# Performance work log

Measured on AMD Instinct MI355X. Metric: run time of the kernel, lower is better.

Reference implementation:

```python
import jax, jax.numpy as jnp
import numpy as np


def setup_inputs() -> dict:
    key = jax.random.key(0)
    k0, k1, k2, k3 = jax.random.split(key, 4)
    B, C = 32, 768
    t_h = t_w = 8
    s_h = s_w = 16
    N = t_h * t_w * 2 + s_h * s_w  # 384
    return {
        "x_v": jax.random.normal(k0, (B, N, C), jnp.float32),
        "x_i": jax.random.normal(k1, (B, N, C), jnp.float32),
        "qkv_w": jax.random.normal(k2, (3 * C, C), jnp.float32) * 0.02,
        "proj_w": jax.random.normal(k3, (C, C), jnp.float32) * 0.02,
        "proj_b": jnp.zeros((C,), jnp.float32),
        "t_h": t_h, "t_w": t_w, "s_h": s_h, "s_w": s_w,
        "num_heads": 12,
    }


def reference(x_v, x_i, qkv_w, proj_w, proj_b, t_h, t_w, s_h, s_w, num_heads):
    B, N, C = x_v.shape
    H = num_heads
    Dh = C // H
    scale = Dh ** (-0.5)
    mt = t_h * t_w * 2  # template tokens (two templates)

    # joint QKV projection over both modalities: [2B, N, C]
    x = jnp.concatenate([x_v, x_i], axis=0)
    qkv = (x @ qkv_w.T).reshape(2 * B, N, 3, H, Dh)
    qkv = jnp.transpose(qkv, (2, 0, 3, 1, 4))  # [3, 2B, H, N, Dh]
    q, k, v = qkv[0], qkv[1], qkv[2]
    qV, qI = q[:B], q[B:]
    kV, kI = k[:B], k[B:]
    vV, vI = v[:B], v[B:]

    q_mt_V, q_s_V = qV[:, :, :mt], qV[:, :, mt:]
    k_mt_V, k_s_V = kV[:, :, :mt], kV[:, :, mt:]
    v_mt_V, v_s_V = vV[:, :, :mt], vV[:, :, mt:]
    q_mt_I, q_s_I = qI[:, :, :mt], qI[:, :, mt:]
    k_mt_I, k_s_I = kI[:, :, :mt], kI[:, :, mt:]
    v_mt_I, v_s_I = vI[:, :, :mt], vI[:, :, mt:]

    # shared cross-modal template KV
    k_mt = jnp.concatenate([k_mt_V, k_mt_I], axis=2)
    v_mt = jnp.concatenate([v_mt_V, v_mt_I], axis=2)

    def attend(q_, k_, v_):
        a = jax.nn.softmax(jnp.einsum('bhqd,bhkd->bhqk', q_, k_) * scale, axis=-1)
        o = jnp.einsum('bhqk,bhkd->bhqd', a, v_)
        return o.transpose(0, 2, 1, 3).reshape(B, -1, C)

    # template branches: self-attention within own modality
    x_mt_V = attend(q_mt_V, k_mt_V, v_mt_V)
    x_mt_I = attend(q_mt_I, k_mt_I, v_mt_I)
    # search branches: attend to cross-modal templates + own search
    x_s_V = attend(q_s_V, jnp.concatenate([k_mt, k_s_V], axis=2),
                   jnp.concatenate([v_mt, v_s_V], axis=2))
    x_s_I = attend(q_s_I, jnp.concatenate([k_mt, k_s_I], axis=2),
                   jnp.concatenate([v_mt, v_s_I], axis=2))

    x_V = jnp.concatenate([x_mt_V, x_s_V], axis=1)
    x_I = jnp.concatenate([x_mt_I, x_s_I], axis=1)
    out = jnp.concatenate([x_V, x_I], axis=0) @ proj_w.T + proj_b
    return out[:B], out[B:]
```

## Files before the change

### kernel.cpp

```cpp
#include <hip/hip_runtime.h>

typedef __bf16 bf16;
typedef __bf16 bf16x4 __attribute__((ext_vector_type(4)));
typedef __bf16 bf16x8 __attribute__((ext_vector_type(8)));
typedef float f32x4 __attribute__((ext_vector_type(4)));

#define MFMA16(a,b,c) __builtin_amdgcn_mfma_f32_16x16x32_bf16((a),(b),(c),0,0,0)
#define SBAR() __builtin_amdgcn_s_barrier()
#define SCHED0() __builtin_amdgcn_sched_barrier(0)
#define EXP2(x) __builtin_amdgcn_exp2f(x)


__device__ inline void gload16(const bf16* g, bf16* l) {
  __builtin_amdgcn_global_load_lds(
      (const __attribute__((address_space(1))) void*)g,
      (__attribute__((address_space(3))) void*)l, 16, 0, 0);
}

__device__ inline void stage128(const bf16* __restrict__ gsrc,
                                bf16* lds_base, int tid, int wv) {
#pragma unroll
  for (int r = 0; r < 4; ++r) {
    int s = r * 256 + tid;
    int row = s >> 3;
    int chunk = (s & 7) ^ (row & 7);
    gload16(gsrc + (size_t)row * 768 + chunk * 8,
            lds_base + (size_t)(r * 256 + wv * 64) * 8);
  }
}

__device__ inline bf16x8 frag64(const bf16* buf, int row, int ks, int lg) {
  int slot = ((ks << 2) | lg) ^ (row & 7);
  return *(const bf16x8*)(buf + (size_t)row * 64 + slot * 8);
}

#define GEMM128_LOOP(APANEL, BPANEL, NTILES)                                    \
  do {                                                                          \
    stage128((APANEL), &As[0][0][0], tid, wv);                                  \
    stage128((BPANEL), &Bs[0][0][0], tid, wv);                                  \
    stage128((APANEL) + 64, &As[1][0][0], tid, wv);                             \
    stage128((BPANEL) + 64, &Bs[1][0][0], tid, wv);                             \
    asm volatile("s_waitcnt vmcnt(8)" ::: "memory"); SCHED0();                  \
    SBAR();                                                                     \
    int c = 0;                                                                  \
    for (int t = 0; t < (NTILES); ++t) {                                        \
      const bf16* Ab = &As[c][0][0];                                            \
      const bf16* Bb = &Bs[c][0][0];                                            \
      bf16x8 af[4][2], bfr[4][2];                                               \
      _Pragma("unroll")                                                         \
      for (int nf = 0; nf < 4; ++nf)                                            \
        _Pragma("unroll")                                                       \
        for (int ks = 0; ks < 2; ++ks)                                          \
          bfr[nf][ks] = frag64(Bb, wc + nf * 16 + lr, ks, lg);                  \
      _Pragma("unroll")                                                         \
      for (int mf = 0; mf < 4; ++mf)                                            \
        _Pragma("unroll")                                                       \
        for (int ks = 0; ks < 2; ++ks)                                          \
          af[mf][ks] = frag64(Ab, wr + mf * 16 + lr, ks, lg);                   \
      asm volatile("s_waitcnt lgkmcnt(0)" ::: "memory"); SCHED0();              \
      SBAR();              \
      if (t + 2 < (NTILES)) {                                                   \
        stage128((APANEL) + (t + 2) * 64, &As[c][0][0], tid, wv);               \
        stage128((BPANEL) + (t + 2) * 64, &Bs[c][0][0], tid, wv);               \
      }                                                                         \
      __builtin_amdgcn_s_setprio(1);                                            \
      _Pragma("unroll")                                                         \
      for (int mf = 0; mf < 4; ++mf)                                            \
        _Pragma("unroll")                                                       \
        for (int nf = 0; nf < 4; ++nf)                                          \
          _Pragma("unroll")                                                     \
          for (int ks = 0; ks < 2; ++ks)                                        \
            acc[mf][nf] = MFMA16(af[mf][ks], bfr[nf][ks], acc[mf][nf]);         \
      __builtin_amdgcn_s_setprio(0);                                            \
      if (t + 2 < (NTILES)) { asm volatile("s_waitcnt vmcnt(8)" ::: "memory"); }\
      else                  { asm volatile("s_waitcnt vmcnt(0)" ::: "memory"); }\
      SCHED0();                                                                 \
      SBAR();                       \
      c ^= 1;                                                                   \
    }                                                                           \
  } while (0)

__global__ __launch_bounds__(256) void convert1_kernel(
    const float* __restrict__ xv, const float* __restrict__ xi,
    const float* __restrict__ w, bf16* __restrict__ dst)
{
  const size_t NV = 9437184;
  const size_t NX = 18874368;
  const size_t NT = 20643840;
  for (size_t i = (size_t)blockIdx.x * 256 + threadIdx.x; i * 8 < NT;
       i += (size_t)gridDim.x * 256) {
    size_t e = i * 8;
    const float* src;
    if (e < NV)      src = xv + e;
    else if (e < NX) src = xi + (e - NV);
    else             src = w + (e - NX);
    f32x4 a = *(const f32x4*)src;
    f32x4 b = *(const f32x4*)(src + 4);
    bf16x8 r;
    r[0] = (bf16)a[0]; r[1] = (bf16)a[1]; r[2] = (bf16)a[2]; r[3] = (bf16)a[3];
    r[4] = (bf16)b[0]; r[5] = (bf16)b[1]; r[6] = (bf16)b[2]; r[7] = (bf16)b[3];
    *(bf16x8*)(dst + e) = r;
  }
}

__global__ __launch_bounds__(256) void convert2_kernel(
    const float* __restrict__ w, bf16* __restrict__ dst)
{
  size_t i = (size_t)blockIdx.x * 256 + threadIdx.x;
  size_t e = i * 8;
  if (e >= 589824) return;
  f32x4 a = *(const f32x4*)(w + e);
  f32x4 b = *(const f32x4*)(w + e + 4);
  bf16x8 r;
  r[0] = (bf16)a[0]; r[1] = (bf16)a[1]; r[2] = (bf16)a[2]; r[3] = (bf16)a[3];
  r[4] = (bf16)b[0]; r[5] = (bf16)b[1]; r[6] = (bf16)b[2]; r[7] = (bf16)b[3];
  *(bf16x8*)(dst + e) = r;
}

__global__ __launch_bounds__(256, 2) void qkv_kernel(
    const bf16* __restrict__ X, const bf16* __restrict__ W,
    bf16* __restrict__ Qo, bf16* __restrict__ Ko, bf16* __restrict__ VTo)
{
  __shared__ union {
    struct { bf16 A[2][128][64]; bf16 B[2][128][64]; } k;
    bf16 ep[128][132];
  } lds;
  bf16 (&As)[2][128][64] = lds.k.A;
  bf16 (&Bs)[2][128][64] = lds.k.B;

  int bid = blockIdx.x;
  int swz = (bid & 7) * 432 + (bid >> 3);
  const int nt = swz % 18, mt = swz / 18;
  const int m0 = mt * 128, n0 = nt * 128;
  const int tid = threadIdx.x;
  const int lane = tid & 63;
  const int wv = tid >> 6;
  const int wr = (wv >> 1) * 64, wc = (wv & 1) * 64;
  const int lr = lane & 15, lg = lane >> 4;

  const bf16* Xp = X + (size_t)m0 * 768;
  const bf16* Wp = W + (size_t)n0 * 768;

  f32x4 acc[4][4] = {};

  GEMM128_LOOP(Xp, Wp, 12);

  const int comp = nt / 6;
  if (comp == 2) {
#pragma unroll
    for (int mf = 0; mf < 4; ++mf)
#pragma unroll
      for (int nf = 0; nf < 4; ++nf) {
        int m = m0 + wr + mf * 16 + lg * 4;
        int n = n0 + wc + nf * 16 + lr;
        int bp = m / 384, tok = m - bp * 384;
        int rem = n - 1536;
        int hh = rem >> 6, d = rem & 63;
        bf16x4 pk;
        pk[0] = (bf16)acc[mf][nf][0]; pk[1] = (bf16)acc[mf][nf][1];
        pk[2] = (bf16)acc[mf][nf][2]; pk[3] = (bf16)acc[mf][nf][3];
        *(bf16x4*)(VTo + (((size_t)bp * 12 + hh) * 64 + d) * 384 + tok) = pk;
      }
  } else {
    const float scl = (comp == 0) ? 0.18033688f : 1.0f;
#pragma unroll
    for (int mf = 0; mf < 4; ++mf)
#pragma unroll
      for (int nf = 0; nf < 4; ++nf)
#pragma unroll
        for (int r = 0; r < 4; ++r)
          lds.ep[wr + mf * 16 + lg * 4 + r][wc + nf * 16 + lr] =
              (bf16)(acc[mf][nf][r] * scl);
    __syncthreads();
    bf16* dst = (comp == 0) ? Qo : Ko;
    const int nb = n0 - comp * 768;
#pragma unroll
    for (int it = 0; it < 8; ++it) {
      int idx = it * 256 + tid;
      int row = idx >> 4, ch = idx & 15;
      int m = m0 + row;
      int bp = m / 384, tok = m - bp * 384;
      int rem = nb + ch * 8;
      int hh = rem >> 6, d = rem & 63;
      *(bf16x8*)(dst + (((size_t)bp * 12 + hh) * 384 + tok) * 64 + d) =
          *(const bf16x8*)(&lds.ep[row][ch * 8]);
    }
  }
}

__global__ __launch_bounds__(256) void attn_kernel(
    const bf16* __restrict__ Q, const bf16* __restrict__ K, const bf16* __restrict__ VT,
    bf16* __restrict__ ATT)
{
  __shared__ union {
    bf16 Qs[128][72];
    bf16 Ps[4][32][136];
  } u;
  __shared__ bf16 Ks[128][72];
  __shared__ bf16 VTs[64][136];

  const int bid = blockIdx.x;
  const int qb = bid % 3;
  const int h  = (bid / 3) % 12;
  const int bp = bid / 36;
  const int tid = threadIdx.x;
  const int lane = tid & 63;
  const int wv = tid >> 6;
  const int lr = lane & 15, lg = lane >> 4;

  const size_t bh384 = ((size_t)bp * 12 + h) * 384;
  const int q0 = qb * 128;
  const int nchunks = (qb == 0) ? 1 : 4;

  auto chunk_base = [&](int c, size_t& kb, size_t& vtb) {
    int src_b, t0;
    if (qb == 0)      { src_b = bp;             t0 = 0; }
    else if (c == 0)  { src_b = bp & 31;        t0 = 0; }
    else if (c == 1)  { src_b = (bp & 31) + 32; t0 = 0; }
    else              { src_b = bp;             t0 = (c - 1) * 128; }
    kb  = (((size_t)src_b * 12 + h) * 384 + t0) * 64;
    vtb = ((size_t)src_b * 12 + h) * 64 * 384 + t0;
  };

  for (int v = tid; v < 1024; v += 256) {
    int row = v >> 3, cg = (v & 7) * 8;
    *(bf16x8*)(&u.Qs[row][cg]) = *(const bf16x8*)(Q + (bh384 + q0 + row) * 64 + cg);
  }
  __syncthreads();

  bf16x8 qf[2][2];
#pragma unroll
  for (int mf = 0; mf < 2; ++mf)
#pragma unroll
    for (int ks = 0; ks < 2; ++ks)
      qf[mf][ks] = *(const bf16x8*)(&u.Qs[wv * 32 + mf * 16 + lr][ks * 32 + lg * 8]);

  const int krow = tid >> 3,  kcg = (tid & 7) * 8;
  const int vd   = tid >> 4,  vp  = (tid & 15) * 8;
  bf16x8 kreg[4], vreg[4];
  {
    size_t kb, vtb; chunk_base(0, kb, vtb);
#pragma unroll
    for (int i = 0; i < 4; ++i) {
      kreg[i] = *(const bf16x8*)(K + kb + (size_t)(krow + i * 32) * 64 + kcg);
      vreg[i] = *(const bf16x8*)(VT + vtb + (size_t)(vd + i * 16) * 384 + vp);
    }
  }

  f32x4 O[2][4] = {};
  float runmax[2] = {-1e30f, -1e30f}, runsum[2] = {0.f, 0.f};

  for (int c = 0; c < nchunks; ++c) {
    __syncthreads();
#pragma unroll
    for (int i = 0; i < 4; ++i) {
      *(bf16x8*)(&Ks[krow + i * 32][kcg]) = kreg[i];
      *(bf16x8*)(&VTs[vd + i * 16][vp])   = vreg[i];
    }
    __syncthreads();

    if (c + 1 < nchunks) {
      size_t kb, vtb; chunk_base(c + 1, kb, vtb);
#pragma unroll
      for (int i = 0; i < 4; ++i) {
        kreg[i] = *(const bf16x8*)(K + kb + (size_t)(krow + i * 32) * 64 + kcg);
        vreg[i] = *(const bf16x8*)(VT + vtb + (size_t)(vd + i * 16) * 384 + vp);
      }
    }

    f32x4 St[2][8] = {};
#pragma unroll
    for (int nf = 0; nf < 8; ++nf) {
#pragma unroll
      for (int ks = 0; ks < 2; ++ks) {
        bf16x8 kf = *(const bf16x8*)(&Ks[nf * 16 + lr][ks * 32 + lg * 8]);
        St[0][nf] = MFMA16(kf, qf[0][ks], St[0][nf]);
        St[1][nf] = MFMA16(kf, qf[1][ks], St[1][nf]);
      }
    }

    float rfq[2];
#pragma unroll
    for (int mf = 0; mf < 2; ++mf) {
      float m4[8];
#pragma unroll
      for (int nf = 0; nf < 8; ++nf)
        m4[nf] = fmaxf(fmaxf(St[mf][nf][0], St[mf][nf][1]),
                       fmaxf(St[mf][nf][2], St[mf][nf][3]));
      float mx = fmaxf(fmaxf(fmaxf(m4[0], m4[1]), fmaxf(m4[2], m4[3])),
                       fmaxf(fmaxf(m4[4], m4[5]), fmaxf(m4[6], m4[7])));
      mx = fmaxf(mx, __shfl_xor(mx, 16));
      mx = fmaxf(mx, __shfl_xor(mx, 32));
      float nm = fmaxf(runmax[mf], mx);
      rfq[mf] = EXP2(runmax[mf] - nm);
      runmax[mf] = nm;
      float s4[8];
#pragma unroll
      for (int nf = 0; nf < 8; ++nf) {
        St[mf][nf][0] = EXP2(St[mf][nf][0] - nm);
        St[mf][nf][1] = EXP2(St[mf][nf][1] - nm);
        St[mf][nf][2] = EXP2(St[mf][nf][2] - nm);
        St[mf][nf][3] = EXP2(St[mf][nf][3] - nm);
        s4[nf] = (St[mf][nf][0] + St[mf][nf][1]) + (St[mf][nf][2] + St[mf][nf][3]);
      }
      float rs = ((s4[0] + s4[1]) + (s4[2] + s4[3])) +
                 ((s4[4] + s4[5]) + (s4[6] + s4[7]));
      rs += __shfl_xor(rs, 16);
      rs += __shfl_xor(rs, 32);
      runsum[mf] = runsum[mf] * rfq[mf] + rs;
    }

#pragma unroll
    for (int mf = 0; mf < 2; ++mf)
#pragma unroll
      for (int nf = 0; nf < 8; ++nf) {
        bf16x4 pk;
        pk[0] = (bf16)St[mf][nf][0]; pk[1] = (bf16)St[mf][nf][1];
        pk[2] = (bf16)St[mf][nf][2]; pk[3] = (bf16)St[mf][nf][3];
        *(bf16x4*)(&u.Ps[wv][mf * 16 + lr][nf * 16 + lg * 4]) = pk;
      }

#pragma unroll
    for (int mf = 0; mf < 2; ++mf)
#pragma unroll
      for (int r = 0; r < 4; ++r) {
        float rr = __shfl(rfq[mf], (lg * 4 + r) + (lg << 4));
#pragma unroll
        for (int vn = 0; vn < 4; ++vn) O[mf][vn][r] *= rr;
      }

#pragma unroll
    for (int ks = 0; ks < 4; ++ks) {
      bf16x8 pf0 = *(const bf16x8*)(&u.Ps[wv][lr][ks * 32 + lg * 8]);
      bf16x8 pf1 = *(const bf16x8*)(&u.Ps[wv][16 + lr][ks * 32 + lg * 8]);
#pragma unroll
      for (int vn = 0; vn < 4; ++vn) {
        bf16x8 vf = *(const bf16x8*)(&VTs[vn * 16 + lr][ks * 32 + lg * 8]);
        O[0][vn] = MFMA16(pf0, vf, O[0][vn]);
        O[1][vn] = MFMA16(pf1, vf, O[1][vn]);
      }
    }
  }

#pragma unroll
  for (int mf = 0; mf < 2; ++mf) {
#pragma unroll
    for (int r = 0; r < 4; ++r) {
      float rs = __shfl(runsum[mf], (lg * 4 + r) + (lg << 4));
      float inv = 1.0f / rs;
#pragma unroll
      for (int vn = 0; vn < 4; ++vn) {
        int tok = q0 + wv * 32 + mf * 16 + lg * 4 + r;
        int d = vn * 16 + lr;
        ATT[((size_t)bp * 384 + tok) * 768 + h * 64 + d] = (bf16)(O[mf][vn][r] * inv);
      }
    }
  }
}

__global__ __launch_bounds__(256, 2) void proj_kernel(
    const bf16* __restrict__ A, const bf16* __restrict__ W,
    const float* __restrict__ bias, float* __restrict__ out)
{
  __shared__ bf16 As[2][128][64];
  __shared__ bf16 Bs[2][128][64];
  int bid = blockIdx.x;
  int swz = (bid & 7) * 144 + (bid >> 3);
  const int nt = swz % 6, mt = swz / 6;
  const int m0 = mt * 128, n0 = nt * 128;
  const int tid = threadIdx.x;
  const int lane = tid & 63;
  const int wv = tid >> 6;
  const int wr = (wv >> 1) * 64, wc = (wv & 1) * 64;
  const int lr = lane & 15, lg = lane >> 4;

  const bf16* Ap = A + (size_t)m0 * 768;
  const bf16* Wpp = W + (size_t)n0 * 768;

  f32x4 acc[4][4] = {};

  GEMM128_LOOP(Ap, Wpp, 12);

#pragma unroll
  for (int mf = 0; mf < 4; ++mf)
#pragma unroll
    for (int nf = 0; nf < 4; ++nf)
#pragma unroll
      for (int r = 0; r < 4; ++r) {
        int m = m0 + wr + mf * 16 + lg * 4 + r;
        int n = n0 + wc + nf * 16 + lr;
        out[(size_t)m * 768 + n] = acc[mf][nf][r] + bias[n];
      }
}

extern "C" void kernel_launch(void* const* d_in, const int* in_sizes, int n_in,
                              void* d_out, int out_size, void* d_ws, size_t ws_size,
                              hipStream_t stream) {
  (void)in_sizes; (void)n_in; (void)out_size; (void)ws_size;
  const float* xv     = (const float*)d_in[0];
  const float* xi     = (const float*)d_in[1];
  const float* qkv_w  = (const float*)d_in[2];
  const float* proj_w = (const float*)d_in[3];
  const float* proj_b = (const float*)d_in[4];
  float* out = (float*)d_out;

  bf16* Xb = (bf16*)d_out;
  bf16* Wq = Xb + (size_t)18874368;

  const size_t SZ = (size_t)64 * 12 * 384 * 64;
  bf16* Q   = (bf16*)d_ws;
  bf16* K   = Q + SZ;
  bf16* VT  = K + SZ;
  bf16* ATT = VT + SZ;
  bf16* Wp  = Q;

  convert1_kernel<<<2048, 256, 0, stream>>>(xv, xi, qkv_w, Xb);
  qkv_kernel<<<3456, 256, 0, stream>>>(Xb, Wq, Q, K, VT);
  attn_kernel<<<64 * 12 * 3, 256, 0, stream>>>(Q, K, VT, ATT);
  convert2_kernel<<<288, 256, 0, stream>>>(proj_w, Wp);
  proj_kernel<<<1152, 256, 0, stream>>>(ATT, Wp, proj_b, out);
}
```

Measured before the change: 244.2 us.

## Fuse fp32-to-bf16 activation conversion into QKV GEMM A-tile loading

```diff
diff --git a/kernel.cpp b/kernel.cpp
--- a/kernel.cpp
+++ b/kernel.cpp
@@ -33,6 +33,27 @@
   int slot = ((ks << 2) | lg) ^ (row & 7);
   return *(const bf16x8*)(buf + (size_t)row * 64 + slot * 8);
 }
+
+#define A_ISSUE(KT)                                                             \
+  _Pragma("unroll")                                                             \
+  for (int i = 0; i < 8; ++i) {                                                 \
+    int s = i * 256 + tid;                                                      \
+    int row = s >> 4, c4 = (s & 15) * 4;                                        \
+    areg[i] = *(const f32x4*)(Asrc + (size_t)row * 768 + (KT) + c4);            \
+  }
+
+#define A_WRITE(BUFA)                                                           \
+  _Pragma("unroll")                                                             \
+  for (int i = 0; i < 8; ++i) {                                                 \
+    int s = i * 256 + tid;                                                      \
+    int row = s >> 4, c4 = (s & 15) * 4;                                        \
+    int slot = (c4 >> 3) ^ (row & 7);                                           \
+    int half = (c4 >> 2) & 1;                                                   \
+    bf16x4 pk;                                                                  \
+    pk[0] = (bf16)areg[i][0]; pk[1] = (bf16)areg[i][1];                         \
+    pk[2] = (bf16)areg[i][2]; pk[3] = (bf16)areg[i][3];                         \
+    *(bf16x4*)((BUFA) + (size_t)row * 64 + slot * 8 + half * 4) = pk;           \
+  }
 
 #define GEMM128_LOOP(APANEL, BPANEL, NTILES)                                    \
   do {                                                                          \
@@ -81,26 +102,17 @@
   } while (0)
 
 __global__ __launch_bounds__(256) void convert1_kernel(
-    const float* __restrict__ xv, const float* __restrict__ xi,
     const float* __restrict__ w, bf16* __restrict__ dst)
 {
-  const size_t NV = 9437184;
-  const size_t NX = 18874368;
-  const size_t NT = 20643840;
-  for (size_t i = (size_t)blockIdx.x * 256 + threadIdx.x; i * 8 < NT;
-       i += (size_t)gridDim.x * 256) {
-    size_t e = i * 8;
-    const float* src;
-    if (e < NV)      src = xv + e;
-    else if (e < NX) src = xi + (e - NV);
-    else             src = w + (e - NX);
-    f32x4 a = *(const f32x4*)src;
-    f32x4 b = *(const f32x4*)(src + 4);
-    bf16x8 r;
-    r[0] = (bf16)a[0]; r[1] = (bf16)a[1]; r[2] = (bf16)a[2]; r[3] = (bf16)a[3];
-    r[4] = (bf16)b[0]; r[5] = (bf16)b[1]; r[6] = (bf16)b[2]; r[7] = (bf16)b[3];
-    *(bf16x8*)(dst + e) = r;
-  }
+  size_t i = (size_t)blockIdx.x * 256 + threadIdx.x;
+  size_t e = i * 8;
+  if (e >= 1769472) return;
+  f32x4 a = *(const f32x4*)(w + e);
+  f32x4 b = *(const f32x4*)(w + e + 4);
+  bf16x8 r;
+  r[0] = (bf16)a[0]; r[1] = (bf16)a[1]; r[2] = (bf16)a[2]; r[3] = (bf16)a[3];
+  r[4] = (bf16)b[0]; r[5] = (bf16)b[1]; r[6] = (bf16)b[2]; r[7] = (bf16)b[3];
+  *(bf16x8*)(dst + e) = r;
 }
 
 __global__ __launch_bounds__(256) void convert2_kernel(
@@ -118,7 +130,8 @@
 }
 
 __global__ __launch_bounds__(256, 2) void qkv_kernel(
-    const bf16* __restrict__ X, const bf16* __restrict__ W,
+    const float* __restrict__ xv, const float* __restrict__ xi,
+    const bf16* __restrict__ W,
     bf16* __restrict__ Qo, bf16* __restrict__ Ko, bf16* __restrict__ VTo)
 {
   __shared__ union {
@@ -138,12 +151,54 @@
   const int wr = (wv >> 1) * 64, wc = (wv & 1) * 64;
   const int lr = lane & 15, lg = lane >> 4;
 
-  const bf16* Xp = X + (size_t)m0 * 768;
+  const float* Asrc = (m0 < 12288) ? (xv + (size_t)m0 * 768)
+                                   : (xi + (size_t)(m0 - 12288) * 768);
   const bf16* Wp = W + (size_t)n0 * 768;
 
   f32x4 acc[4][4] = {};
-
-  GEMM128_LOOP(Xp, Wp, 12);
+  f32x4 areg[8];
+
+  A_ISSUE(0);
+  stage128(Wp, &Bs[0][0][0], tid, wv);
+  stage128(Wp + 64, &Bs[1][0][0], tid, wv);
+  A_WRITE(&As[0][0][0]);
+  asm volatile("s_waitcnt vmcnt(4)" ::: "memory"); SCHED0();
+  asm volatile("s_waitcnt lgkmcnt(0)" ::: "memory"); SCHED0();
+  SBAR();
+
+  int c = 0;
+  for (int t = 0; t < 12; ++t) {
+    if (t + 1 < 12) A_ISSUE((t + 1) * 64);
+    const bf16* Ab = &As[c][0][0];
+    const bf16* Bb = &Bs[c][0][0];
+    bf16x8 af[4][2], bfr[4][2];
+#pragma unroll
+    for (int nf = 0; nf < 4; ++nf)
+#pragma unroll
+      for (int ks = 0; ks < 2; ++ks)
+        bfr[nf][ks] = frag64(Bb, wc + nf * 16 + lr, ks, lg);
+#pragma unroll
+    for (int mf = 0; mf < 4; ++mf)
+#pragma unroll
+      for (int ks = 0; ks < 2; ++ks)
+        af[mf][ks] = frag64(Ab, wr + mf * 16 + lr, ks, lg);
+    asm volatile("s_waitcnt lgkmcnt(0)" ::: "memory"); SCHED0();
+    SBAR();
+    if (t + 2 < 12) stage128(Wp + (t + 2) * 64, &Bs[c][0][0], tid, wv);
+    __builtin_amdgcn_s_setprio(1);
+#pragma unroll
+    for (int mf = 0; mf < 4; ++mf)
+#pragma unroll
+      for (int nf = 0; nf < 4; ++nf)
+#pragma unroll
+        for (int ks = 0; ks < 2; ++ks)
+          acc[mf][nf] = MFMA16(af[mf][ks], bfr[nf][ks], acc[mf][nf]);
+    __builtin_amdgcn_s_setprio(0);
+    if (t + 1 < 12) A_WRITE(&As[c ^ 1][0][0]);
+    asm volatile("s_waitcnt lgkmcnt(0)" ::: "memory"); SCHED0();
+    SBAR();
+    c ^= 1;
+  }
 
   const int comp = nt / 6;
   if (comp == 2) {
@@ -404,8 +459,7 @@
   const float* proj_b = (const float*)d_in[4];
   float* out = (float*)d_out;
 
-  bf16* Xb = (bf16*)d_out;
-  bf16* Wq = Xb + (size_t)18874368;
+  bf16* Wq = (bf16*)d_out;
 
   const size_t SZ = (size_t)64 * 12 * 384 * 64;
   bf16* Q   = (bf16*)d_ws;
@@ -414,8 +468,8 @@
   bf16* ATT = VT + SZ;
   bf16* Wp  = Q;
 
-  convert1_kernel<<<2048, 256, 0, stream>>>(xv, xi, qkv_w, Xb);
-  qkv_kernel<<<3456, 256, 0, stream>>>(Xb, Wq, Q, K, VT);
+  convert1_kernel<<<864, 256, 0, stream>>>(qkv_w, Wq);
+  qkv_kernel<<<3456, 256, 0, stream>>>(xv, xi, Wq, Q, K, VT);
   attn_kernel<<<64 * 12 * 3, 256, 0, stream>>>(Q, K, VT, ATT);
   convert2_kernel<<<288, 256, 0, stream>>>(proj_w, Wp);
   proj_kernel<<<1152, 256, 0, stream>>>(ATT, Wp, proj_b, out);
```

After: 282.5 us. +15.7%, slower.
